# Optimization experiments

Hardware: AMD Instinct MI355X
Metric: run time of the kernel (lower is better)

The kernel has to match this reference:

```python
import jax, jax.numpy as jnp
import numpy as np

EMBED_DIM = 2048
NUM_HEADS = 32
HEAD_DIM = EMBED_DIM // NUM_HEADS
SCALE = HEAD_DIM ** -0.5
B, S = 2, 2048


def setup_inputs() -> dict:
    key = jax.random.key(0)
    ks = jax.random.split(key, 9)
    std = EMBED_DIM ** -0.5
    inp = {
        "h": jax.random.normal(ks[0], (B, S, EMBED_DIM), dtype=jnp.float32),
        "Wq": jax.random.normal(ks[1], (EMBED_DIM, EMBED_DIM), dtype=jnp.float32) * std,
        "bq": jax.random.normal(ks[2], (EMBED_DIM,), dtype=jnp.float32) * 0.02,
        "Wk": jax.random.normal(ks[3], (EMBED_DIM, EMBED_DIM), dtype=jnp.float32) * std,
        "bk": jax.random.normal(ks[4], (EMBED_DIM,), dtype=jnp.float32) * 0.02,
        "Wv": jax.random.normal(ks[5], (EMBED_DIM, EMBED_DIM), dtype=jnp.float32) * std,
        "bv": jax.random.normal(ks[6], (EMBED_DIM,), dtype=jnp.float32) * 0.02,
        "Wo": jax.random.normal(ks[7], (EMBED_DIM, EMBED_DIM), dtype=jnp.float32) * std,
        "bo": jax.random.normal(ks[8], (EMBED_DIM,), dtype=jnp.float32) * 0.02,
    }
    return inp


def reference(h, Wq, bq, Wk, bk, Wv, bv, Wo, bo):
    # QKV projections (nn.Linear: x @ W.T + b)
    q = h @ Wq.T + bq  # [B, S, E]
    k = h @ Wk.T + bk
    v = h @ Wv.T + bv
    # split heads
    q = q.reshape(B, S, NUM_HEADS, HEAD_DIM)
    k = k.reshape(B, S, NUM_HEADS, HEAD_DIM)
    v = v.reshape(B, S, NUM_HEADS, HEAD_DIM)
    # scaled dot-product attention with causal (tril) mask
    scores = jnp.einsum("bqhd,bkhd->bhqk", q, k) * SCALE  # [B, H, S, S]
    causal = jnp.tril(jnp.ones((S, S), dtype=bool))  # [S, S]
    neg = jnp.finfo(scores.dtype).min
    scores = jnp.where(causal[None, None, :, :], scores, neg)
    attn = jax.nn.softmax(scores, axis=-1)
    o = jnp.einsum("bhqk,bkhd->bqhd", attn, v).reshape(B, S, EMBED_DIM)
    return o @ Wo.T + bo
```

## Files before the change

kernel.cpp:

```cpp
#include <hip/hip_runtime.h>
#include <hip/hip_bf16.h>
#include <stdint.h>

#define EMBED 2048
#define NHEADS 32
#define HDIM 64
#define BATCH 2
#define SEQ 2048
#define ATT_SCALE 0.125f
#define LOG2E 1.4426950408889634f

typedef __attribute__((ext_vector_type(8))) short bf16x8;
typedef __attribute__((ext_vector_type(4))) float f32x4;
typedef __attribute__((ext_vector_type(16))) float f32x16;
typedef __attribute__((ext_vector_type(4))) unsigned short u16x4;
typedef __attribute__((ext_vector_type(2))) unsigned int u32x2;

static __device__ __forceinline__ unsigned short f2bf(float f) {
  union { float f; uint32_t u; } v; v.f = f;
  uint32_t r = v.u + 0x7fffu + ((v.u >> 16) & 1u);
  return (unsigned short)(r >> 16);
}

static __device__ __forceinline__ void gload_lds16(const unsigned short* g, unsigned short* l) {
  __builtin_amdgcn_global_load_lds(
      (const __attribute__((address_space(1))) unsigned int*)g,
      (__attribute__((address_space(3))) unsigned int*)l, 16, 0, 0);
}

__global__ void cvt_all(const float* __restrict__ h,
                        const float* __restrict__ Wq, const float* __restrict__ Wk,
                        const float* __restrict__ Wv, const float* __restrict__ Wo,
                        unsigned short* __restrict__ out) {
  const int n4 = 6291456;
  int idx = blockIdx.x * blockDim.x + threadIdx.x;
  int stride = gridDim.x * blockDim.x;
  for (int i = idx; i < n4; i += stride) {
    const float* src; int off;
    if (i < 2097152)      { src = h;  off = i; }
    else if (i < 3145728) { src = Wq; off = i - 2097152; }
    else if (i < 4194304) { src = Wk; off = i - 3145728; }
    else if (i < 5242880) { src = Wv; off = i - 4194304; }
    else                  { src = Wo; off = i - 5242880; }
    float4 v = ((const float4*)src)[off];
    u16x4 o;
    o.x = f2bf(v.x); o.y = f2bf(v.y); o.z = f2bf(v.z); o.w = f2bf(v.w);
    ((u16x4*)out)[i] = o;
  }
}

__global__ __launch_bounds__(256, 2)
void gemm_qkv(const unsigned short* __restrict__ A,
              const unsigned short* __restrict__ W,
              const float* __restrict__ biasq, const float* __restrict__ biask,
              const float* __restrict__ biasv,
              unsigned short* __restrict__ Qo, unsigned short* __restrict__ Ko,
              unsigned short* __restrict__ Vo, float qscale) {
  __shared__ unsigned short A_lds[128 * 64];
  __shared__ unsigned short B_lds[128 * 64];
  const int tid = threadIdx.x;
  const int w = tid >> 6, l = tid & 63;
  const int wr = w >> 1, wc = w & 1;
  const int r16 = l & 15, g = l >> 4;
  const int bi = blockIdx.x / 48, bj = blockIdx.x % 48;
  const int row0 = bi * 128, col0 = bj * 128;

  f32x4 acc[4][4];
#pragma unroll
  for (int i = 0; i < 4; ++i)
#pragma unroll
    for (int j = 0; j < 4; ++j) acc[i][j] = (f32x4){0.f, 0.f, 0.f, 0.f};

  const int srow = tid >> 3;
  const int scol = (tid & 7) * 8;

  for (int kt = 0; kt < 32; ++kt) {
    const int k0 = kt * 64;
#pragma unroll
    for (int j = 0; j < 4; ++j)
      gload_lds16(A + (size_t)(row0 + j * 32 + srow) * 2048 + k0 + scol,
                  A_lds + j * 2048 + w * 512);
#pragma unroll
    for (int j = 0; j < 4; ++j)
      gload_lds16(W + (size_t)(col0 + j * 32 + srow) * 2048 + k0 + scol,
                  B_lds + j * 2048 + w * 512);
    __syncthreads();
#pragma unroll
    for (int ks = 0; ks < 2; ++ks) {
      bf16x8 af[4], bfr[4];
#pragma unroll
      for (int mf = 0; mf < 4; ++mf)
        af[mf] = *(const bf16x8*)(A_lds + (wr * 64 + mf * 16 + r16) * 64 + ks * 32 + g * 8);
#pragma unroll
      for (int nf = 0; nf < 4; ++nf)
        bfr[nf] = *(const bf16x8*)(B_lds + (wc * 64 + nf * 16 + r16) * 64 + ks * 32 + g * 8);
#pragma unroll
      for (int mf = 0; mf < 4; ++mf)
#pragma unroll
        for (int nf = 0; nf < 4; ++nf)
          acc[mf][nf] = __builtin_amdgcn_mfma_f32_16x16x32_bf16(af[mf], bfr[nf], acc[mf][nf], 0, 0, 0);
    }
    __syncthreads();
  }

  const int which = col0 >> 11;
  const float* bb = (which == 0) ? biasq : (which == 1) ? biask : biasv;
  const float osc = (which == 0) ? qscale : 1.0f;
  unsigned short* outp = (which == 0) ? Qo : (which == 1) ? Ko : Vo;
#pragma unroll
  for (int mf = 0; mf < 4; ++mf) {
    const int irow = row0 + wr * 64 + mf * 16 + g * 4;
#pragma unroll
    for (int nf = 0; nf < 4; ++nf) {
      const int jcol = col0 + wc * 64 + nf * 16 + r16;
      const int jl = jcol & 2047;
      const int hh = jl >> 6, d = jl & 63;
      const float bval = bb[jl];
#pragma unroll
      for (int r = 0; r < 4; ++r) {
        const float val = (acc[mf][nf][r] + bval) * osc;
        const int i = irow + r;
        const int b = i >> 11, s = i & 2047;
        size_t off;
        if (which < 2) off = (((size_t)(b * NHEADS + hh)) * SEQ + s) * HDIM + d;
        else           off = (((size_t)(b * NHEADS + hh)) * HDIM + d) * SEQ + s;
        outp[off] = f2bf(val);
      }
    }
  }
}

__global__ __launch_bounds__(256, 2)
void gemm_out(const unsigned short* __restrict__ A,
              const unsigned short* __restrict__ W,
              const float* __restrict__ bias,
              float* __restrict__ out) {
  __shared__ unsigned short A_lds[128 * 64];
  __shared__ unsigned short B_lds[128 * 64];
  const int tid = threadIdx.x;
  const int w = tid >> 6, l = tid & 63;
  const int wr = w >> 1, wc = w & 1;
  const int r16 = l & 15, g = l >> 4;
  const int bi = blockIdx.x >> 4, bj = blockIdx.x & 15;
  const int row0 = bi * 128, col0 = bj * 128;

  f32x4 acc[4][4];
#pragma unroll
  for (int i = 0; i < 4; ++i)
#pragma unroll
    for (int j = 0; j < 4; ++j) acc[i][j] = (f32x4){0.f, 0.f, 0.f, 0.f};

  const int srow = tid >> 3;
  const int scol = (tid & 7) * 8;

  for (int kt = 0; kt < 32; ++kt) {
    const int k0 = kt * 64;
#pragma unroll
    for (int j = 0; j < 4; ++j)
      gload_lds16(A + (size_t)(row0 + j * 32 + srow) * 2048 + k0 + scol,
                  A_lds + j * 2048 + w * 512);
#pragma unroll
    for (int j = 0; j < 4; ++j)
      gload_lds16(W + (size_t)(col0 + j * 32 + srow) * 2048 + k0 + scol,
                  B_lds + j * 2048 + w * 512);
    __syncthreads();
#pragma unroll
    for (int ks = 0; ks < 2; ++ks) {
      bf16x8 af[4], bfr[4];
#pragma unroll
      for (int mf = 0; mf < 4; ++mf)
        af[mf] = *(const bf16x8*)(A_lds + (wr * 64 + mf * 16 + r16) * 64 + ks * 32 + g * 8);
#pragma unroll
      for (int nf = 0; nf < 4; ++nf)
        bfr[nf] = *(const bf16x8*)(B_lds + (wc * 64 + nf * 16 + r16) * 64 + ks * 32 + g * 8);
#pragma unroll
      for (int mf = 0; mf < 4; ++mf)
#pragma unroll
        for (int nf = 0; nf < 4; ++nf)
          acc[mf][nf] = __builtin_amdgcn_mfma_f32_16x16x32_bf16(af[mf], bfr[nf], acc[mf][nf], 0, 0, 0);
    }
    __syncthreads();
  }

#pragma unroll
  for (int mf = 0; mf < 4; ++mf) {
    const int irow = row0 + wr * 64 + mf * 16 + g * 4;
#pragma unroll
    for (int nf = 0; nf < 4; ++nf) {
      const int jcol = col0 + wc * 64 + nf * 16 + r16;
      const float bval = bias[jcol];
#pragma unroll
      for (int r = 0; r < 4; ++r)
        out[(size_t)(irow + r) * 2048 + jcol] = acc[mf][nf][r] + bval;
    }
  }
}

__global__ __launch_bounds__(256, 2)
void attn_kernel(const unsigned short* __restrict__ Q,
                 const unsigned short* __restrict__ K,
                 const unsigned short* __restrict__ Vt,
                 unsigned short* __restrict__ O) {
  __shared__ unsigned short K_lds[2][64 * 72];
  __shared__ unsigned short V_lds[2][64 * 72];
  __shared__ __align__(16) float abuf[4][32];
  __shared__ __align__(16) float lbuf[4][32];
  const int tid = threadIdx.x;
  const int w = tid >> 6, l = tid & 63;
  const int q5 = l & 31, hi = l >> 5;
  const int bid = ((blockIdx.x & 7) << 6) | (blockIdx.x >> 3);
  const int pair = bid & 7;
  const int bh = bid >> 3;
  const unsigned short* Qh = Q + (size_t)bh * SEQ * HDIM;
  const unsigned short* Kh = K + (size_t)bh * SEQ * HDIM;
  const unsigned short* Vh = Vt + (size_t)bh * HDIM * SEQ;
  const int bq = bh >> 5, hh = bh & 31;
  const int srow = tid >> 3;
  const int scol = (tid & 7) * 8;

  for (int half = 0; half < 2; ++half) {
    const int qt = half ? (15 - pair) : pair;
    const int wrow0 = qt * 128 + w * 32;
    const int wrow_max = wrow0 + 31;
    const int n_tiles = 2 * qt + 2;
    const int qrow = wrow0 + q5;

    bf16x8 qf[4];
#pragma unroll
    for (int ks = 0; ks < 4; ++ks)
      qf[ks] = *(const bf16x8*)(Qh + (size_t)qrow * HDIM + ks * 16 + hi * 8);

    f32x16 oacc[2];
#pragma unroll
    for (int df = 0; df < 2; ++df)
#pragma unroll
      for (int r = 0; r < 16; ++r) oacc[df][r] = 0.f;
    float m_run = -3.0e38f, l_run = 0.f;

    bf16x8 kreg[2], vreg[2];
#pragma unroll
    for (int j = 0; j < 2; ++j) {
      const int rr = j * 32 + srow;
      kreg[j] = *(const bf16x8*)(Kh + (size_t)rr * HDIM + scol);
      vreg[j] = *(const bf16x8*)(Vh + (size_t)rr * SEQ + scol);
    }
    __syncthreads();
#pragma unroll
    for (int j = 0; j < 2; ++j) {
      const int rr = j * 32 + srow;
      *(bf16x8*)(K_lds[0] + rr * 72 + scol) = kreg[j];
      *(bf16x8*)(V_lds[0] + rr * 72 + scol) = vreg[j];
    }

    for (int t = 0; t < n_tiles; ++t) {
      const int cur = t & 1;
      const bool not_last = (t + 1 < n_tiles);
      if (not_last) {
#pragma unroll
        for (int j = 0; j < 2; ++j) {
          const int rr = j * 32 + srow;
          kreg[j] = *(const bf16x8*)(Kh + (size_t)((t + 1) * 64 + rr) * HDIM + scol);
          vreg[j] = *(const bf16x8*)(Vh + (size_t)rr * SEQ + (t + 1) * 64 + scol);
        }
      }
      __syncthreads();

      if (t * 64 <= wrow_max) {
        f32x16 skf[2];
#pragma unroll
        for (int kf = 0; kf < 2; ++kf)
#pragma unroll
          for (int r = 0; r < 16; ++r) skf[kf][r] = 0.f;
        __builtin_amdgcn_s_setprio(1);
#pragma unroll
        for (int kf = 0; kf < 2; ++kf)
#pragma unroll
          for (int ks = 0; ks < 4; ++ks) {
            bf16x8 ak = *(const bf16x8*)(K_lds[cur] + (kf * 32 + q5) * 72 + ks * 16 + hi * 8);
            skf[kf] = __builtin_amdgcn_mfma_f32_32x32x16_bf16(ak, qf[ks], skf[kf], 0, 0, 0);
          }
        __builtin_amdgcn_s_setprio(0);

        const bool need_mask = (t * 64 + 63 > wrow0);
        if (need_mask) {
#pragma unroll
          for (int kf = 0; kf < 2; ++kf)
#pragma unroll
            for (int r = 0; r < 16; ++r) {
              const int key = t * 64 + kf * 32 + (r & 3) + 8 * (r >> 2) + 4 * hi;
              if (key > qrow) skf[kf][r] = -3.0e38f;
            }
        }

        float mx = -3.0e38f;
#pragma unroll
        for (int kf = 0; kf < 2; ++kf)
#pragma unroll
          for (int r = 0; r < 16; ++r) mx = fmaxf(mx, skf[kf][r]);
        mx = fmaxf(mx, __shfl_xor(mx, 32));

        if (__any(mx > m_run + 8.0f)) {
          const float mnew = fmaxf(m_run, mx);
          const float alpha = exp2f(m_run - mnew);
          m_run = mnew;
          l_run *= alpha;
          if (l < 32) abuf[w][l] = alpha;
          f32x4 av[4];
#pragma unroll
          for (int k = 0; k < 4; ++k)
            av[k] = *(const f32x4*)&abuf[w][8 * k + 4 * hi];
#pragma unroll
          for (int df = 0; df < 2; ++df)
#pragma unroll
            for (int r = 0; r < 16; ++r) oacc[df][r] *= av[r >> 2][r & 3];
        }

        unsigned int pkA[8], pkB[8];
        float psum = 0.f;
#pragma unroll
        for (int kf = 0; kf < 2; ++kf)
#pragma unroll
          for (int rr = 0; rr < 4; ++rr) {
            unsigned int pb[4];
#pragma unroll
            for (int j = 0; j < 4; ++j) {
              const float p = exp2f(skf[kf][rr * 4 + j] - m_run);
              psum += p;
              union { float f; unsigned int u; } c; c.f = p;
              pb[j] = c.u + 0x8000u;
            }
            pkA[kf * 4 + rr] = __builtin_amdgcn_perm(pb[1], pb[0], 0x07060302);
            pkB[kf * 4 + rr] = __builtin_amdgcn_perm(pb[3], pb[2], 0x07060302);
          }
        psum += __shfl_xor(psum, 32);
        l_run += psum;

        __builtin_amdgcn_s_setprio(1);
#pragma unroll
        for (int ks = 0; ks < 4; ++ks) {
          u32x2 ra = __builtin_amdgcn_permlane32_swap(pkA[2 * ks], pkA[2 * ks + 1], false, false);
          u32x2 rb = __builtin_amdgcn_permlane32_swap(pkB[2 * ks], pkB[2 * ks + 1], false, false);
          union { unsigned int u[4]; bf16x8 v; } pa;
          pa.u[0] = ra.x; pa.u[1] = rb.x; pa.u[2] = ra.y; pa.u[3] = rb.y;
#pragma unroll
          for (int df = 0; df < 2; ++df) {
            bf16x8 vf = *(const bf16x8*)(V_lds[cur] + (df * 32 + q5) * 72 + ks * 16 + hi * 8);
            oacc[df] = __builtin_amdgcn_mfma_f32_32x32x16_bf16(pa.v, vf, oacc[df], 0, 0, 0);
          }
        }
        __builtin_amdgcn_s_setprio(0);
      }

      if (not_last) {
#pragma unroll
        for (int j = 0; j < 2; ++j) {
          const int rr = j * 32 + srow;
          *(bf16x8*)(K_lds[cur ^ 1] + rr * 72 + scol) = kreg[j];
          *(bf16x8*)(V_lds[cur ^ 1] + rr * 72 + scol) = vreg[j];
        }
      }
    }

    if (l < 32) lbuf[w][l] = l_run;
    f32x4 lv[4];
#pragma unroll
    for (int k = 0; k < 4; ++k)
      lv[k] = *(const f32x4*)&lbuf[w][8 * k + 4 * hi];
#pragma unroll
    for (int df = 0; df < 2; ++df) {
      const int d = df * 32 + q5;
#pragma unroll
      for (int r = 0; r < 16; ++r) {
        const int s = wrow0 + (r & 3) + 8 * (r >> 2) + 4 * hi;
        const float inv = __builtin_amdgcn_rcpf(lv[r >> 2][r & 3]);
        O[((size_t)(bq * SEQ + s)) * EMBED + hh * HDIM + d] = f2bf(oacc[df][r] * inv);
      }
    }
  }
}

extern "C" void kernel_launch(void* const* d_in, const int* in_sizes, int n_in,
                              void* d_out, int out_size, void* d_ws, size_t ws_size,
                              hipStream_t stream) {
  const float* h  = (const float*)d_in[0];
  const float* Wq = (const float*)d_in[1];
  const float* bq = (const float*)d_in[2];
  const float* Wk = (const float*)d_in[3];
  const float* bk = (const float*)d_in[4];
  const float* Wv = (const float*)d_in[5];
  const float* bv = (const float*)d_in[6];
  const float* Wo = (const float*)d_in[7];
  const float* bo = (const float*)d_in[8];

  if (ws_size < (size_t)117440512) return;

  unsigned short* ws = (unsigned short*)d_ws;
  unsigned short* hb = ws;
  unsigned short* wqb = ws + 8388608;
  unsigned short* wob = ws + 20971520;
  unsigned short* Qw  = ws + 25165824;
  unsigned short* Kw  = ws + 33554432;
  unsigned short* Vw  = ws + 41943040;
  unsigned short* Ow  = ws + 50331648;

  cvt_all<<<2048, 256, 0, stream>>>(h, Wq, Wk, Wv, Wo, ws);

  const float qscale = ATT_SCALE * LOG2E;
  gemm_qkv<<<1536, 256, 0, stream>>>(hb, wqb, bq, bk, bv, Qw, Kw, Vw, qscale);

  attn_kernel<<<512, 256, 0, stream>>>(Qw, Kw, Vw, Ow);

  gemm_out<<<512, 256, 0, stream>>>(Ow, wob, bo, (float*)d_out);
}
```

Before: 274.9 us.

## Replace GEMMs with 256x128 double-buffered pipelined templated kernel

Both projection GEMMs are merged into one templated kernel that uses 512-thread blocks and 256x128 tiles. The K loop is double-buffered in LDS, with global-to-LDS staging for the next tiles interleaved between MFMA quarters. It adds an XOR swizzle on LDS columns to avoid bank conflicts, an L2-friendly block-index swizzle, and s_setprio around the MFMA groups. The aim is to hide global load latency and raise MFMA utilisation. In exchange it uses more LDS per block (96 KB) and relies on hand-tuned vmcnt waits and barriers.

New measurement: 246.0 us. 10.5% less time.

```diff
diff --git a/kernel.cpp b/kernel.cpp
--- a/kernel.cpp
+++ b/kernel.cpp
@@ -49,21 +49,24 @@
   }
 }
 
-__global__ __launch_bounds__(256, 2)
-void gemm_qkv(const unsigned short* __restrict__ A,
-              const unsigned short* __restrict__ W,
-              const float* __restrict__ biasq, const float* __restrict__ biask,
-              const float* __restrict__ biasv,
-              unsigned short* __restrict__ Qo, unsigned short* __restrict__ Ko,
-              unsigned short* __restrict__ Vo, float qscale) {
-  __shared__ unsigned short A_lds[128 * 64];
-  __shared__ unsigned short B_lds[128 * 64];
+template<int MODE, int NBJ>
+__global__ __launch_bounds__(512, 2)
+void gemm8(const unsigned short* __restrict__ A,
+           const unsigned short* __restrict__ W,
+           const float* __restrict__ b0, const float* __restrict__ b1,
+           const float* __restrict__ b2,
+           unsigned short* __restrict__ o0, unsigned short* __restrict__ o1,
+           unsigned short* __restrict__ o2,
+           float* __restrict__ fo, float qscale) {
+  __shared__ unsigned short lds[2][24576];
   const int tid = threadIdx.x;
   const int w = tid >> 6, l = tid & 63;
-  const int wr = w >> 1, wc = w & 1;
+  const int wm = w >> 1, wn = w & 1;
   const int r16 = l & 15, g = l >> 4;
-  const int bi = blockIdx.x / 48, bj = blockIdx.x % 48;
-  const int row0 = bi * 128, col0 = bj * 128;
+  const int nblk = 16 * NBJ;
+  const int swz = (blockIdx.x & 7) * (nblk >> 3) + (blockIdx.x >> 3);
+  const int bi = swz / NBJ, bj = swz % NBJ;
+  const int arow0 = bi * 256, bcol0 = bj * 128;
 
   f32x4 acc[4][4];
 #pragma unroll
@@ -71,127 +74,111 @@
 #pragma unroll
     for (int j = 0; j < 4; ++j) acc[i][j] = (f32x4){0.f, 0.f, 0.f, 0.f};
 
-  const int srow = tid >> 3;
-  const int scol = (tid & 7) * 8;
-
-  for (int kt = 0; kt < 32; ++kt) {
-    const int k0 = kt * 64;
-#pragma unroll
-    for (int j = 0; j < 4; ++j)
-      gload_lds16(A + (size_t)(row0 + j * 32 + srow) * 2048 + k0 + scol,
-                  A_lds + j * 2048 + w * 512);
-#pragma unroll
-    for (int j = 0; j < 4; ++j)
-      gload_lds16(W + (size_t)(col0 + j * 32 + srow) * 2048 + k0 + scol,
-                  B_lds + j * 2048 + w * 512);
-    __syncthreads();
-#pragma unroll
-    for (int ks = 0; ks < 2; ++ks) {
-      bf16x8 af[4], bfr[4];
-#pragma unroll
-      for (int mf = 0; mf < 4; ++mf)
-        af[mf] = *(const bf16x8*)(A_lds + (wr * 64 + mf * 16 + r16) * 64 + ks * 32 + g * 8);
-#pragma unroll
-      for (int nf = 0; nf < 4; ++nf)
-        bfr[nf] = *(const bf16x8*)(B_lds + (wc * 64 + nf * 16 + r16) * 64 + ks * 32 + g * 8);
-#pragma unroll
-      for (int mf = 0; mf < 4; ++mf)
-#pragma unroll
-        for (int nf = 0; nf < 4; ++nf)
-          acc[mf][nf] = __builtin_amdgcn_mfma_f32_16x16x32_bf16(af[mf], bfr[nf], acc[mf][nf], 0, 0, 0);
-    }
-    __syncthreads();
+  const int lrow = l >> 3;
+  const int gcu = ((l & 7) ^ lrow) * 8;
+
+  auto stageA = [&](int buf, int t, int mq, int call) {
+    const int m = call * 8 + w;
+    const int row0 = mq * 32 + (m >> 2) * 64 + (m & 3) * 8;
+    gload_lds16(A + (size_t)(arow0 + row0 + lrow) * 2048 + t * 64 + gcu,
+                &lds[buf][row0 * 64]);
+  };
+  auto stageB = [&](int buf, int t, int nq) {
+    const int row0 = nq * 32 + (w >> 2) * 64 + (w & 3) * 8;
+    gload_lds16(W + (size_t)(bcol0 + row0 + lrow) * 2048 + t * 64 + gcu,
+                &lds[buf][16384 + row0 * 64]);
+  };
+  auto ldA = [&](int buf, int mf, int ks) -> bf16x8 {
+    const int row = wm * 64 + mf * 16 + r16;
+    const int u = (ks * 4 + g) ^ (r16 & 7);
+    return *(const bf16x8*)&lds[buf][row * 64 + u * 8];
+  };
+  auto ldB = [&](int buf, int nf, int ks) -> bf16x8 {
+    const int row = wn * 64 + nf * 16 + r16;
+    const int u = (ks * 4 + g) ^ (r16 & 7);
+    return *(const bf16x8*)&lds[buf][16384 + row * 64 + u * 8];
+  };
+
+  stageA(0, 0, 0, 0); stageA(0, 0, 0, 1); stageB(0, 0, 0);
+  stageA(0, 0, 1, 0); stageA(0, 0, 1, 1); stageB(0, 0, 1);
+  stageA(1, 1, 0, 0); stageA(1, 1, 0, 1); stageB(1, 1, 0);
+  asm volatile("s_waitcnt vmcnt(3)" ::: "memory");
+  __builtin_amdgcn_sched_barrier(0);
+  __builtin_amdgcn_s_barrier();
+
+  bf16x8 af[2][2], bf[4][2];
+
+#define MMA_Q(MQ, NQ)                                                          \
+  __builtin_amdgcn_s_setprio(1);                                               \
+  _Pragma("unroll")                                                            \
+  for (int i = 0; i < 2; ++i)                                                  \
+    _Pragma("unroll")                                                          \
+    for (int j = 0; j < 2; ++j)                                                \
+      _Pragma("unroll")                                                        \
+      for (int ks = 0; ks < 2; ++ks)                                           \
+        acc[(MQ)*2 + i][(NQ)*2 + j] = __builtin_amdgcn_mfma_f32_16x16x32_bf16( \
+            af[i][ks], bf[(NQ)*2 + j][ks], acc[(MQ)*2 + i][(NQ)*2 + j], 0, 0, 0); \
+  __builtin_amdgcn_s_setprio(0);
+
+  const int nt = 32;
+  for (int c = 0; c < nt; ++c) {
+    const int X = c & 1;
+    const bool s1 = (c + 1 < nt), s2 = (c + 2 < nt);
+    af[0][0] = ldA(X, 0, 0); af[0][1] = ldA(X, 0, 1);
+    af[1][0] = ldA(X, 1, 0); af[1][1] = ldA(X, 1, 1);
+    bf[0][0] = ldB(X, 0, 0); bf[0][1] = ldB(X, 0, 1);
+    bf[1][0] = ldB(X, 1, 0); bf[1][1] = ldB(X, 1, 1);
+    if (s1) { stageA(X ^ 1, c + 1, 1, 0); stageA(X ^ 1, c + 1, 1, 1); }
+    MMA_Q(0, 0);
+    __builtin_amdgcn_s_barrier();
+    bf[2][0] = ldB(X, 2, 0); bf[2][1] = ldB(X, 2, 1);
+    bf[3][0] = ldB(X, 3, 0); bf[3][1] = ldB(X, 3, 1);
+    if (s1) stageB(X ^ 1, c + 1, 1);
+    MMA_Q(0, 1);
+    __builtin_amdgcn_s_barrier();
+    af[0][0] = ldA(X, 2, 0); af[0][1] = ldA(X, 2, 1);
+    af[1][0] = ldA(X, 3, 0); af[1][1] = ldA(X, 3, 1);
+    if (s2) { stageA(X, c + 2, 0, 0); stageA(X, c + 2, 0, 1); }
+    MMA_Q(1, 0);
+    __builtin_amdgcn_s_barrier();
+    if (s2) stageB(X, c + 2, 0);
+    MMA_Q(1, 1);
+    if (s2) asm volatile("s_waitcnt vmcnt(3)" ::: "memory");
+    else    asm volatile("s_waitcnt vmcnt(0)" ::: "memory");
+    __builtin_amdgcn_sched_barrier(0);
+    __builtin_amdgcn_s_barrier();
   }
-
-  const int which = col0 >> 11;
-  const float* bb = (which == 0) ? biasq : (which == 1) ? biask : biasv;
-  const float osc = (which == 0) ? qscale : 1.0f;
-  unsigned short* outp = (which == 0) ? Qo : (which == 1) ? Ko : Vo;
+#undef MMA_Q
+
 #pragma unroll
   for (int mf = 0; mf < 4; ++mf) {
-    const int irow = row0 + wr * 64 + mf * 16 + g * 4;
+    const int irow = arow0 + wm * 64 + mf * 16 + g * 4;
 #pragma unroll
     for (int nf = 0; nf < 4; ++nf) {
-      const int jcol = col0 + wc * 64 + nf * 16 + r16;
-      const int jl = jcol & 2047;
-      const int hh = jl >> 6, d = jl & 63;
-      const float bval = bb[jl];
-#pragma unroll
-      for (int r = 0; r < 4; ++r) {
-        const float val = (acc[mf][nf][r] + bval) * osc;
-        const int i = irow + r;
-        const int b = i >> 11, s = i & 2047;
-        size_t off;
-        if (which < 2) off = (((size_t)(b * NHEADS + hh)) * SEQ + s) * HDIM + d;
-        else           off = (((size_t)(b * NHEADS + hh)) * HDIM + d) * SEQ + s;
-        outp[off] = f2bf(val);
+      const int jcol = bcol0 + wn * 64 + nf * 16 + r16;
+      if (MODE == 1) {
+        const float bval = b0[jcol];
+#pragma unroll
+        for (int rr = 0; rr < 4; ++rr)
+          fo[(size_t)(irow + rr) * 2048 + jcol] = acc[mf][nf][rr] + bval;
+      } else {
+        const int which = bj >> 4;
+        const int jl = jcol & 2047;
+        const int hh = jl >> 6, d = jl & 63;
+        const float bval = (which == 0) ? b0[jl] : (which == 1) ? b1[jl] : b2[jl];
+        const float osc = (which == 0) ? qscale : 1.0f;
+        unsigned short* outp = (which == 0) ? o0 : (which == 1) ? o1 : o2;
+#pragma unroll
+        for (int rr = 0; rr < 4; ++rr) {
+          const float val = (acc[mf][nf][rr] + bval) * osc;
+          const int i = irow + rr;
+          const int b = i >> 11, s = i & 2047;
+          size_t off;
+          if (which < 2) off = (((size_t)(b * NHEADS + hh)) * SEQ + s) * HDIM + d;
+          else           off = (((size_t)(b * NHEADS + hh)) * HDIM + d) * SEQ + s;
+          outp[off] = f2bf(val);
+        }
       }
-    }
-  }
-}
-
-__global__ __launch_bounds__(256, 2)
-void gemm_out(const unsigned short* __restrict__ A,
-              const unsigned short* __restrict__ W,
-              const float* __restrict__ bias,
-              float* __restrict__ out) {
-  __shared__ unsigned short A_lds[128 * 64];
-  __shared__ unsigned short B_lds[128 * 64];
-  const int tid = threadIdx.x;
-  const int w = tid >> 6, l = tid & 63;
-  const int wr = w >> 1, wc = w & 1;
-  const int r16 = l & 15, g = l >> 4;
-  const int bi = blockIdx.x >> 4, bj = blockIdx.x & 15;
-  const int row0 = bi * 128, col0 = bj * 128;
-
-  f32x4 acc[4][4];
-#pragma unroll
-  for (int i = 0; i < 4; ++i)
-#pragma unroll
-    for (int j = 0; j < 4; ++j) acc[i][j] = (f32x4){0.f, 0.f, 0.f, 0.f};
-
-  const int srow = tid >> 3;
-  const int scol = (tid & 7) * 8;
-
-  for (int kt = 0; kt < 32; ++kt) {
-    const int k0 = kt * 64;
-#pragma unroll
-    for (int j = 0; j < 4; ++j)
-      gload_lds16(A + (size_t)(row0 + j * 32 + srow) * 2048 + k0 + scol,
-                  A_lds + j * 2048 + w * 512);
-#pragma unroll
-    for (int j = 0; j < 4; ++j)
-      gload_lds16(W + (size_t)(col0 + j * 32 + srow) * 2048 + k0 + scol,
-                  B_lds + j * 2048 + w * 512);
-    __syncthreads();
-#pragma unroll
-    for (int ks = 0; ks < 2; ++ks) {
-      bf16x8 af[4], bfr[4];
-#pragma unroll
-      for (int mf = 0; mf < 4; ++mf)
-        af[mf] = *(const bf16x8*)(A_lds + (wr * 64 + mf * 16 + r16) * 64 + ks * 32 + g * 8);
-#pragma unroll
-      for (int nf = 0; nf < 4; ++nf)
-        bfr[nf] = *(const bf16x8*)(B_lds + (wc * 64 + nf * 16 + r16) * 64 + ks * 32 + g * 8);
-#pragma unroll
-      for (int mf = 0; mf < 4; ++mf)
-#pragma unroll
-        for (int nf = 0; nf < 4; ++nf)
-          acc[mf][nf] = __builtin_amdgcn_mfma_f32_16x16x32_bf16(af[mf], bfr[nf], acc[mf][nf], 0, 0, 0);
-    }
-    __syncthreads();
-  }
-
-#pragma unroll
-  for (int mf = 0; mf < 4; ++mf) {
-    const int irow = row0 + wr * 64 + mf * 16 + g * 4;
-#pragma unroll
-    for (int nf = 0; nf < 4; ++nf) {
-      const int jcol = col0 + wc * 64 + nf * 16 + r16;
-      const float bval = bias[jcol];
-#pragma unroll
-      for (int r = 0; r < 4; ++r)
-        out[(size_t)(irow + r) * 2048 + jcol] = acc[mf][nf][r] + bval;
     }
   }
 }
@@ -406,9 +393,10 @@
   cvt_all<<<2048, 256, 0, stream>>>(h, Wq, Wk, Wv, Wo, ws);
 
   const float qscale = ATT_SCALE * LOG2E;
-  gemm_qkv<<<1536, 256, 0, stream>>>(hb, wqb, bq, bk, bv, Qw, Kw, Vw, qscale);
+  gemm8<0, 48><<<768, 512, 0, stream>>>(hb, wqb, bq, bk, bv, Qw, Kw, Vw, nullptr, qscale);
 
   attn_kernel<<<512, 256, 0, stream>>>(Qw, Kw, Vw, Ow);
 
-  gemm_out<<<512, 256, 0, stream>>>(Ow, wob, bo, (float*)d_out);
-}
+  gemm8<1, 16><<<256, 512, 0, stream>>>(Ow, wob, bo, bo, bo, nullptr, nullptr, nullptr,
+                                        (float*)d_out, 1.0f);
+}
```
